# Kernel tuning notes

Hardware: AMD Instinct MI355X
Metric: run time of the kernel (lower is better)

## Reference

```python
import jax, jax.numpy as jnp
import numpy as np

EPS = 1e-6

def _layernorm(x, gamma, beta):
    # normalize over last dim (head_dim)
    mean = x.mean(axis=-1, keepdims=True)
    var = x.var(axis=-1, keepdims=True)
    return gamma * (x - mean) * jax.lax.rsqrt(var + EPS) + beta

def setup_inputs() -> dict:
    key = jax.random.key(0)
    ks = jax.random.split(key, 6)
    B, N, C, H = 2, 2048, 1024, 16
    Dh = C // H
    x = jax.random.normal(ks[0], (B, N, C), dtype=jnp.float32)
    qkv_w = jax.random.normal(ks[1], (C, 3 * C), dtype=jnp.float32) * (1.0 / np.sqrt(C))
    q_gamma = jnp.ones((Dh,), jnp.float32)
    q_beta = jnp.zeros((Dh,), jnp.float32)
    k_gamma = jnp.ones((Dh,), jnp.float32)
    k_beta = jnp.zeros((Dh,), jnp.float32)
    proj_w = jax.random.normal(ks[2], (C, C), dtype=jnp.float32) * (1.0 / np.sqrt(C))
    proj_b = jnp.zeros((C,), jnp.float32)
    return {"x": x, "qkv_w": qkv_w, "q_gamma": q_gamma, "q_beta": q_beta,
            "k_gamma": k_gamma, "k_beta": k_beta, "proj_w": proj_w, "proj_b": proj_b}

def reference(x, qkv_w, q_gamma, q_beta, k_gamma, k_beta, proj_w, proj_b):
    B, N, C = x.shape
    H = 16
    Dh = C // H
    scale = Dh ** -0.5
    qkv = x @ qkv_w                                   # [B,N,3C]
    qkv = qkv.reshape(B, N, 3, H, Dh)
    q = qkv[:, :, 0].transpose(0, 2, 1, 3)            # [B,H,N,Dh]
    k = qkv[:, :, 1].transpose(0, 2, 1, 3)
    v = qkv[:, :, 2].transpose(0, 2, 1, 3)
    q = _layernorm(q, q_gamma, q_beta)
    k = _layernorm(k, k_gamma, k_beta)
    attn = jnp.einsum('bhnd,bhmd->bhnm', q, k) * scale
    attn = jax.nn.softmax(attn, axis=-1)
    out = jnp.einsum('bhnm,bhmd->bhnd', attn, v)      # [B,H,N,Dh]
    out = out.transpose(0, 2, 1, 3).reshape(B, N, C)
    return out @ proj_w + proj_b
```

## Files before the change

### kernel.cpp

```cpp
#include <hip/hip_runtime.h>

typedef unsigned short u16;
typedef unsigned int u32;
typedef float f32x4 __attribute__((ext_vector_type(4)));
typedef float f32x16 __attribute__((ext_vector_type(16)));
typedef short s16x8 __attribute__((ext_vector_type(8)));

#define B_ 2
#define N_ 2048
#define C_ 1024
#define H_ 16
#define BN_ (B_*N_)

#define EXP2F(x) __builtin_amdgcn_exp2f(x)

__device__ __forceinline__ u16 f2bf(float f) {
  union { float f; unsigned u; } c; c.f = f;
  unsigned u = c.u;
  u = (u + 0x7fffu + ((u >> 16) & 1u)) >> 16;
  return (u16)u;
}
__device__ __forceinline__ float bf2f(u16 h) {
  union { unsigned u; float f; } c; c.u = ((unsigned)h) << 16;
  return c.f;
}
__device__ __forceinline__ u32 pack2(float lo, float hi) {
  u32 r;
  asm("v_cvt_pk_bf16_f32 %0, %1, %2" : "=v"(r) : "v"(lo), "v"(hi));
  return r;
}
__device__ __forceinline__ void plswap(u32& a, u32& b) {
  asm volatile("v_permlane32_swap_b32 %0, %1" : "+v"(a), "+v"(b));
}
__device__ __forceinline__ void gload16(const u16* g, u16* l) {
  __builtin_amdgcn_global_load_lds(
      (const __attribute__((address_space(1))) unsigned*)g,
      (__attribute__((address_space(3))) unsigned*)l, 16, 0, 0);
}

__global__ __launch_bounds__(256) void k_prep(const float* __restrict__ x,
                                              u16* __restrict__ xb,
                                              const float* __restrict__ qkv_w,
                                              u16* __restrict__ wqkvT,
                                              const float* __restrict__ proj_w,
                                              u16* __restrict__ wprojT) {
  __shared__ float t[32][33];
  int bid = blockIdx.x;
  int tid = threadIdx.x;
  if (bid < 4096) {
    int i = bid * 256 + tid;
    float4 v = ((const float4*)x)[i];
    ushort4 r;
    r.x = f2bf(v.x); r.y = f2bf(v.y); r.z = f2bf(v.z); r.w = f2bf(v.w);
    ((ushort4*)xb)[i] = r;
    return;
  }
  const float* W; u16* Wt; int R, Cc, bx, by;
  if (bid < 7168) {
    int b = bid - 4096;
    bx = b % 96; by = b / 96;
    W = qkv_w; Wt = wqkvT; R = C_; Cc = 3 * C_;
  } else {
    int b = bid - 7168;
    bx = b & 31; by = b >> 5;
    W = proj_w; Wt = wprojT; R = C_; Cc = C_;
  }
  int tx = tid & 31, ty = tid >> 5;
  int c0 = bx * 32, r0 = by * 32;
#pragma unroll
  for (int i = 0; i < 4; ++i)
    t[ty + i * 8][tx] = W[(long)(r0 + ty + i * 8) * Cc + c0 + tx];
  __syncthreads();
#pragma unroll
  for (int i = 0; i < 4; ++i)
    Wt[(long)(c0 + ty + i * 8) * R + r0 + tx] = f2bf(t[tx][ty + i * 8]);
}

__global__ __launch_bounds__(256) void k_gemm_qkv_ln(const u16* __restrict__ A,
                                                     const u16* __restrict__ Bt,
                                                     const float* __restrict__ qg,
                                                     const float* __restrict__ qbeta,
                                                     const float* __restrict__ kg,
                                                     const float* __restrict__ kbeta,
                                                     u16* __restrict__ Qh,
                                                     u16* __restrict__ Kh,
                                                     u16* __restrict__ Vt) {
  const int K = C_;
  __shared__ u16 smem[32768];
  int tid = threadIdx.x;
  int w = tid >> 6, l = tid & 63;
  int l15 = l & 15, lhi = l >> 4;
  int wm = w >> 1, wn = w & 1;
  int rowA = l >> 3;
  int colA = ((l & 7) ^ (rowA & 7)) * 8;
  int x0 = (lhi ^ (l15 & 7)) * 8;
  int x1 = ((4 + lhi) ^ (l15 & 7)) * 8;
  const u16* Ab = A + (long)blockIdx.y * 128 * K;
  const u16* Bb = Bt + (long)blockIdx.x * 128 * K;
  f32x4 acc[4][4];
#pragma unroll
  for (int m = 0; m < 4; ++m)
#pragma unroll
    for (int n = 0; n < 4; ++n)
      acc[m][n] = (f32x4){0.f, 0.f, 0.f, 0.f};

  auto STAGE = [&](int k0, int bi) {
    u16* at = smem + bi * 8192;
    u16* bt = smem + 16384 + bi * 8192;
#pragma unroll
    for (int i = 0; i < 4; ++i) {
      int ci = i * 4 + w;
      gload16(Ab + (long)(ci * 8 + rowA) * K + k0 + colA, &at[ci * 512]);
      gload16(Bb + (long)(ci * 8 + rowA) * K + k0 + colA, &bt[ci * 512]);
    }
  };

  const int NS = K / 64;
  STAGE(0, 0);
  for (int t = 0; t < NS; ++t) {
    __builtin_amdgcn_s_barrier();
    if (t + 1 < NS) {
      STAGE((t + 1) * 64, (t + 1) & 1);
      asm volatile("s_waitcnt vmcnt(8)" ::: "memory");
    } else {
      asm volatile("s_waitcnt vmcnt(0)" ::: "memory");
    }
    __builtin_amdgcn_s_barrier();
    const u16* at = smem + (t & 1) * 8192;
    const u16* bt = smem + 16384 + (t & 1) * 8192;
#pragma unroll
    for (int kk = 0; kk < 2; ++kk) {
      int xo = kk ? x1 : x0;
      s16x8 af[4], bfr[4];
#pragma unroll
      for (int m = 0; m < 4; ++m)
        af[m] = *(const s16x8*)&at[(wm * 64 + m * 16 + l15) * 64 + xo];
#pragma unroll
      for (int n = 0; n < 4; ++n)
        bfr[n] = *(const s16x8*)&bt[(wn * 64 + n * 16 + l15) * 64 + xo];
#pragma unroll
      for (int m = 0; m < 4; ++m)
#pragma unroll
        for (int n = 0; n < 4; ++n)
          acc[m][n] = __builtin_amdgcn_mfma_f32_16x16x32_bf16(af[m], bfr[n], acc[m][n], 0, 0, 0);
    }
  }

  int cb = blockIdx.x * 128 + wn * 64;
  int s = cb >> 10;
  int h = (cb & 1023) >> 6;
  int rowbase = blockIdx.y * 128 + wm * 64;

  if (s == 2) {
    __syncthreads();
    u16* tbuf = smem + w * 4608;
    u32* tb32 = (u32*)tbuf;
#pragma unroll
    for (int m = 0; m < 4; ++m)
#pragma unroll
      for (int n = 0; n < 4; ++n) {
        int d = n * 16 + l15;
#pragma unroll
        for (int r = 0; r < 4; r += 2)
          tb32[d * 36 + m * 8 + lhi * 2 + (r >> 1)] =
              pack2(acc[m][n][r], acc[m][n][r + 1]);
      }
    int b = rowbase >> 11;
    int nnb = rowbase & (N_ - 1);
    int bhv = b * H_ + h;
    int ch = (l & 7) * 8;
#pragma unroll
    for (int i = 0; i < 8; ++i) {
      int dl = i * 8 + (l >> 3);
      s16x8 vv = *(const s16x8*)&tbuf[dl * 72 + ch];
      *(s16x8*)&Vt[(long)(bhv * 64 + dl) * N_ + nnb + ch] = vv;
    }
  } else {
    const float* g = (s == 0) ? qg : kg;
    const float* be = (s == 0) ? qbeta : kbeta;
    u16* Oh = (s == 0) ? Qh : Kh;
    float sc = (s == 0) ? 0.125f * 1.44269504089f : 1.f;
    float gv[4], bv[4];
#pragma unroll
    for (int n = 0; n < 4; ++n) { gv[n] = g[n * 16 + l15]; bv[n] = be[n * 16 + l15]; }
#pragma unroll
    for (int m = 0; m < 4; ++m) {
#pragma unroll
      for (int r = 0; r < 4; ++r) {
        float t = (acc[m][0][r] + acc[m][1][r]) + (acc[m][2][r] + acc[m][3][r]);
        t += __shfl_xor(t, 1); t += __shfl_xor(t, 2);
        t += __shfl_xor(t, 4); t += __shfl_xor(t, 8);
        float mean = t * (1.f / 64.f);
        float v0 = acc[m][0][r] - mean, v1 = acc[m][1][r] - mean;
        float v2 = acc[m][2][r] - mean, v3 = acc[m][3][r] - mean;
        float q2 = (v0 * v0 + v1 * v1) + (v2 * v2 + v3 * v3);
        q2 += __shfl_xor(q2, 1); q2 += __shfl_xor(q2, 2);
        q2 += __shfl_xor(q2, 4); q2 += __shfl_xor(q2, 8);
        float rs = rsqrtf(q2 * (1.f / 64.f) + 1e-6f);
        int row = rowbase + m * 16 + lhi * 4 + r;
        int b = row >> 11, nn = row & (N_ - 1);
        long ob = ((long)(b * H_ + h) * N_ + nn) * 64;
        float vv[4] = {v0, v1, v2, v3};
#pragma unroll
        for (int n = 0; n < 4; ++n)
          Oh[ob + n * 16 + l15] = f2bf(sc * (gv[n] * vv[n] * rs + bv[n]));
      }
    }
  }
}

__global__ __launch_bounds__(256) void k_gemm_proj(const u16* __restrict__ A,
                                                   const u16* __restrict__ Bt,
                                                   float* __restrict__ Cout,
                                                   const float* __restrict__ bias,
                                                   int M, int N, int K) {
  __shared__ u16 a_t[2][128 * 64];
  __shared__ u16 b_t[2][64 * 64];
  int tid = threadIdx.x;
  int w = tid >> 6, l = tid & 63;
  int l15 = l & 15, lhi = l >> 4;
  int rowA = l >> 3;
  int colA = ((l & 7) ^ (rowA & 7)) * 8;
  int x0 = (lhi ^ (l15 & 7)) * 8;
  int x1 = ((4 + lhi) ^ (l15 & 7)) * 8;
  const u16* Ab = A + (long)blockIdx.y * 128 * K;
  const u16* Bb = Bt + (long)blockIdx.x * 64 * K;
  f32x4 acc[2][4];
#pragma unroll
  for (int m = 0; m < 2; ++m)
#pragma unroll
    for (int n = 0; n < 4; ++n)
      acc[m][n] = (f32x4){0.f, 0.f, 0.f, 0.f};

  auto STAGE = [&](int k0, int bi) {
#pragma unroll
    for (int i = 0; i < 4; ++i) {
      int ci = i * 4 + w;
      gload16(Ab + (long)(ci * 8 + rowA) * K + k0 + colA, &a_t[bi][ci * 512]);
    }
#pragma unroll
    for (int i = 0; i < 2; ++i) {
      int ci = i * 4 + w;
      gload16(Bb + (long)(ci * 8 + rowA) * K + k0 + colA, &b_t[bi][ci * 512]);
    }
  };

  const int NS = 1024 / 64;
  STAGE(0, 0);
  for (int t = 0; t < NS; ++t) {
    __builtin_amdgcn_s_barrier();
    if (t + 1 < NS) {
      STAGE((t + 1) * 64, (t + 1) & 1);
      asm volatile("s_waitcnt vmcnt(6)" ::: "memory");
    } else {
      asm volatile("s_waitcnt vmcnt(0)" ::: "memory");
    }
    __builtin_amdgcn_s_barrier();
    const u16* at = a_t[t & 1];
    const u16* bt = b_t[t & 1];
#pragma unroll
    for (int kk = 0; kk < 2; ++kk) {
      int xo = kk ? x1 : x0;
      s16x8 af[2], bfr[4];
#pragma unroll
      for (int m = 0; m < 2; ++m)
        af[m] = *(const s16x8*)&at[(w * 32 + m * 16 + l15) * 64 + xo];
#pragma unroll
      for (int n = 0; n < 4; ++n)
        bfr[n] = *(const s16x8*)&bt[(n * 16 + l15) * 64 + xo];
#pragma unroll
      for (int m = 0; m < 2; ++m)
#pragma unroll
        for (int n = 0; n < 4; ++n)
          acc[m][n] = __builtin_amdgcn_mfma_f32_16x16x32_bf16(af[m], bfr[n], acc[m][n], 0, 0, 0);
    }
  }
#pragma unroll
  for (int m = 0; m < 2; ++m) {
#pragma unroll
    for (int n = 0; n < 4; ++n) {
      int col = blockIdx.x * 64 + n * 16 + l15;
#pragma unroll
      for (int r = 0; r < 4; ++r) {
        int row = blockIdx.y * 128 + w * 32 + m * 16 + lhi * 4 + r;
        Cout[(long)row * N + col] = acc[m][n][r] + bias[col];
      }
    }
  }
}

__global__ __launch_bounds__(512, 4) void k_attn(const u16* __restrict__ Qh,
                                                 const u16* __restrict__ Kh,
                                                 const u16* __restrict__ Vt,
                                                 u16* __restrict__ O) {
  __shared__ u16 k_t[2][2][64 * 64];
  __shared__ u16 v_t[2][2][64 * 64];
  int tid = threadIdx.x;
  int w = tid >> 6, l = tid & 63;
  int half = w >> 2, wq = w & 3;
  int l31 = l & 31, hi = l >> 5;
  int id = blockIdx.x;
  int swz = (id & 7) * 64 + (id >> 3);
  int bh = swz >> 4, qb = swz & 15;
  int b = bh >> 4, h = bh & 15;
  const u16* Qb = Qh + ((long)bh * N_ + qb * 128 + wq * 32) * 64;
  const u16* Kb = Kh + ((long)bh * N_ + half * 1024) * 64;
  const u16* Vb = Vt + (long)bh * 64 * N_ + half * 1024;

  s16x8 qf[4];
#pragma unroll
  for (int j = 0; j < 4; ++j)
    qf[j] = *(const s16x8*)&Qb[l31 * 64 + j * 16 + hi * 8];

  f32x16 acc0, acc1;
#pragma unroll
  for (int i = 0; i < 16; ++i) { acc0[i] = 0.f; acc1[i] = 0.f; }
  float lsum = 0.f;

  int off[2][4];
#pragma unroll
  for (int t = 0; t < 2; ++t)
#pragma unroll
    for (int j = 0; j < 4; ++j)
      off[t][j] = (t * 32 + l31) * 64 + (((j * 2 + hi) ^ (l & 7)) * 8);

  int srow = l >> 3;
  int scol = ((l & 7) ^ srow) * 8;

  auto STAGE = [&](int kt, int bi) {
#pragma unroll
    for (int i = 0; i < 2; ++i) {
      int ci = i * 4 + wq;
      gload16(Kb + (long)(kt + ci * 8 + srow) * 64 + scol, &k_t[half][bi][ci * 512]);
      gload16(Vb + (long)(ci * 8 + srow) * N_ + kt + scol, &v_t[half][bi][ci * 512]);
    }
  };

  const int NT = 16;
  STAGE(0, 0);

  for (int t = 0; t < NT; ++t) {
    __builtin_amdgcn_s_barrier();
    if (t + 1 < NT) {
      STAGE((t + 1) * 64, (t + 1) & 1);
      asm volatile("s_waitcnt vmcnt(4)" ::: "memory");
    } else {
      asm volatile("s_waitcnt vmcnt(0)" ::: "memory");
    }
    __builtin_amdgcn_s_barrier();
    const u16* kb = k_t[half][t & 1];
    const u16* vb = v_t[half][t & 1];

    f32x16 s0, s1;
#pragma unroll
    for (int i = 0; i < 16; ++i) { s0[i] = 0.f; s1[i] = 0.f; }
    __builtin_amdgcn_s_setprio(1);
#pragma unroll
    for (int j = 0; j < 4; ++j) {
      s16x8 kf0 = *(const s16x8*)&kb[off[0][j]];
      s0 = __builtin_amdgcn_mfma_f32_32x32x16_bf16(kf0, qf[j], s0, 0, 0, 0);
      s16x8 kf1 = *(const s16x8*)&kb[off[1][j]];
      s1 = __builtin_amdgcn_mfma_f32_32x32x16_bf16(kf1, qf[j], s1, 0, 0, 0);
    }
    __builtin_amdgcn_s_setprio(0);

#pragma unroll
    for (int i = 0; i < 16; ++i) {
      s0[i] = EXP2F(s0[i]);
      s1[i] = EXP2F(s1[i]);
    }
    f32x16 sm;
#pragma unroll
    for (int i = 0; i < 16; ++i) sm[i] = s0[i] + s1[i];
#pragma unroll
    for (int i = 0; i < 8; ++i) sm[i] += sm[i + 8];
#pragma unroll
    for (int i = 0; i < 4; ++i) sm[i] += sm[i + 4];
    lsum += (sm[0] + sm[1]) + (sm[2] + sm[3]);

    s16x8 pa[4];
#pragma unroll
    for (int g = 0; g < 4; ++g) {
      const f32x16& sv = (g < 2) ? s0 : s1;
      int o = (g & 1) * 8;
      u32 a = pack2(sv[o + 0], sv[o + 1]);
      u32 bb = pack2(sv[o + 4], sv[o + 5]);
      u32 c = pack2(sv[o + 2], sv[o + 3]);
      u32 d = pack2(sv[o + 6], sv[o + 7]);
      plswap(a, bb);
      plswap(c, d);
      union { u32 u[4]; s16x8 v; } fr;
      fr.u[0] = a; fr.u[1] = c; fr.u[2] = bb; fr.u[3] = d;
      pa[g] = fr.v;
    }

    __builtin_amdgcn_s_setprio(1);
#pragma unroll
    for (int j = 0; j < 4; ++j) {
      s16x8 vf0 = *(const s16x8*)&vb[off[0][j]];
      acc0 = __builtin_amdgcn_mfma_f32_32x32x16_bf16(pa[j], vf0, acc0, 0, 0, 0);
      s16x8 vf1 = *(const s16x8*)&vb[off[1][j]];
      acc1 = __builtin_amdgcn_mfma_f32_32x32x16_bf16(pa[j], vf1, acc1, 0, 0, 0);
    }
    __builtin_amdgcn_s_setprio(0);
  }

  lsum += __shfl_xor(lsum, 32);

  __syncthreads();
  float* mbuf = (float*)&k_t[0][0][0];
  float* ml   = (float*)&v_t[0][0][0];

  if (half == 1) {
    if (hi == 0) ml[wq * 32 + l31] = lsum;
#pragma unroll
    for (int r = 0; r < 16; ++r) {
      mbuf[((wq * 32 + r) * 64) + l] = acc0[r];
      mbuf[((wq * 32 + 16 + r) * 64) + l] = acc1[r];
    }
  }
  __syncthreads();

  if (half == 0) {
    float s_b = ml[wq * 32 + l31];
    float lstar = lsum + s_b;
    int lsi = __float_as_int(lstar);
#pragma unroll
    for (int r = 0; r < 16; ++r) {
      int ql = (r & 3) + 8 * (r >> 2) + 4 * hi;
      float ls = __int_as_float(__builtin_amdgcn_ds_bpermute(ql << 2, lsi));
      float o0 = acc0[r] + mbuf[((wq * 32 + r) * 64) + l];
      float o1 = acc1[r] + mbuf[((wq * 32 + 16 + r) * 64) + l];
      float inv = 1.f / ls;
      int q = qb * 128 + wq * 32 + ql;
      long ob = ((long)(b * N_ + q) * H_ + h) * 64 + l31;
      O[ob] = f2bf(o0 * inv);
      O[ob + 32] = f2bf(o1 * inv);
    }
  }
}

extern "C" void kernel_launch(void* const* d_in, const int* in_sizes, int n_in,
                              void* d_out, int out_size, void* d_ws, size_t ws_size,
                              hipStream_t stream) {
  const float* x      = (const float*)d_in[0];
  const float* qkv_w  = (const float*)d_in[1];
  const float* q_g    = (const float*)d_in[2];
  const float* q_b    = (const float*)d_in[3];
  const float* k_g    = (const float*)d_in[4];
  const float* k_b    = (const float*)d_in[5];
  const float* proj_w = (const float*)d_in[6];
  const float* proj_b = (const float*)d_in[7];
  float* out = (float*)d_out;

  char* ws = (char*)d_ws;
  u16* xb     = (u16*)(ws + 0);
  u16* wqkvT  = (u16*)(ws + 8388608);
  u16* wprojT = (u16*)(ws + 14680064);
  u16* Qh     = (u16*)(ws + 16777216);
  u16* Kh     = (u16*)(ws + 25165824);
  u16* Vt     = (u16*)(ws + 41943040);
  u16* attnO  = xb;

  k_prep<<<8192, 256, 0, stream>>>(x, xb, qkv_w, wqkvT, proj_w, wprojT);
  k_gemm_qkv_ln<<<dim3(24, 32), 256, 0, stream>>>(xb, wqkvT, q_g, q_b, k_g, k_b, Qh, Kh, Vt);
  k_attn<<<512, 512, 0, stream>>>(Qh, Kh, Vt, attnO);
  k_gemm_proj<<<dim3(16, 32), 256, 0, stream>>>(attnO, wprojT, out, proj_b, BN_, C_, C_);
}
```

Before: 112.8 us.

## Drop key-split in attention kernel; each wave processes full key range

The attention kernel no longer splits the key sequence across two half-blocks of 4 waves each. It now uses 256 threads per block, and each wave iterates over all 32 key tiles. This removes the cross-half reduction through shared memory, its two __syncthreads, and halves the LDS footprint, which could raise occupancy. In exchange each block runs a serial loop twice as long with half the waves, which gives less latency hiding per block. There is also a cosmetic change to the projection GEMM's LDS indexing.

```diff
diff --git a/kernel.cpp b/kernel.cpp
--- a/kernel.cpp
+++ b/kernel.cpp
@@ -264,7 +264,7 @@
       s16x8 af[2], bfr[4];
 #pragma unroll
       for (int m = 0; m < 2; ++m)
-        af[m] = *(const s16x8*)&at[(w * 32 + m * 16 + l15) * 64 + xo];
+        af[m] = *(const s16x8*)&a_t[t & 1][(w * 32 + m * 16 + l15) * 64 + xo];
 #pragma unroll
       for (int n = 0; n < 4; ++n)
         bfr[n] = *(const s16x8*)&bt[(n * 16 + l15) * 64 + xo];
@@ -273,6 +273,7 @@
 #pragma unroll
         for (int n = 0; n < 4; ++n)
           acc[m][n] = __builtin_amdgcn_mfma_f32_16x16x32_bf16(af[m], bfr[n], acc[m][n], 0, 0, 0);
+      (void)at;
     }
   }
 #pragma unroll
@@ -289,23 +290,22 @@
   }
 }
 
-__global__ __launch_bounds__(512, 4) void k_attn(const u16* __restrict__ Qh,
+__global__ __launch_bounds__(256, 4) void k_attn(const u16* __restrict__ Qh,
                                                  const u16* __restrict__ Kh,
                                                  const u16* __restrict__ Vt,
                                                  u16* __restrict__ O) {
-  __shared__ u16 k_t[2][2][64 * 64];
-  __shared__ u16 v_t[2][2][64 * 64];
+  __shared__ u16 k_t[2][64 * 64];
+  __shared__ u16 v_t[2][64 * 64];
   int tid = threadIdx.x;
   int w = tid >> 6, l = tid & 63;
-  int half = w >> 2, wq = w & 3;
   int l31 = l & 31, hi = l >> 5;
   int id = blockIdx.x;
   int swz = (id & 7) * 64 + (id >> 3);
   int bh = swz >> 4, qb = swz & 15;
   int b = bh >> 4, h = bh & 15;
-  const u16* Qb = Qh + ((long)bh * N_ + qb * 128 + wq * 32) * 64;
-  const u16* Kb = Kh + ((long)bh * N_ + half * 1024) * 64;
-  const u16* Vb = Vt + (long)bh * 64 * N_ + half * 1024;
+  const u16* Qb = Qh + ((long)bh * N_ + qb * 128 + w * 32) * 64;
+  const u16* Kb = Kh + (long)bh * N_ * 64;
+  const u16* Vb = Vt + (long)bh * 64 * N_;
 
   s16x8 qf[4];
 #pragma unroll
@@ -330,13 +330,13 @@
   auto STAGE = [&](int kt, int bi) {
 #pragma unroll
     for (int i = 0; i < 2; ++i) {
-      int ci = i * 4 + wq;
-      gload16(Kb + (long)(kt + ci * 8 + srow) * 64 + scol, &k_t[half][bi][ci * 512]);
-      gload16(Vb + (long)(ci * 8 + srow) * N_ + kt + scol, &v_t[half][bi][ci * 512]);
+      int ci = i * 4 + w;
+      gload16(Kb + (long)(kt + ci * 8 + srow) * 64 + scol, &k_t[bi][ci * 512]);
+      gload16(Vb + (long)(ci * 8 + srow) * N_ + kt + scol, &v_t[bi][ci * 512]);
     }
   };
 
-  const int NT = 16;
+  const int NT = N_ / 64;
   STAGE(0, 0);
 
   for (int t = 0; t < NT; ++t) {
@@ -348,8 +348,8 @@
       asm volatile("s_waitcnt vmcnt(0)" ::: "memory");
     }
     __builtin_amdgcn_s_barrier();
-    const u16* kb = k_t[half][t & 1];
-    const u16* vb = v_t[half][t & 1];
+    const u16* kb = k_t[t & 1];
+    const u16* vb = v_t[t & 1];
 
     f32x16 s0, s1;
 #pragma unroll
@@ -406,37 +406,16 @@
   }
 
   lsum += __shfl_xor(lsum, 32);
-
-  __syncthreads();
-  float* mbuf = (float*)&k_t[0][0][0];
-  float* ml   = (float*)&v_t[0][0][0];
-
-  if (half == 1) {
-    if (hi == 0) ml[wq * 32 + l31] = lsum;
-#pragma unroll
-    for (int r = 0; r < 16; ++r) {
-      mbuf[((wq * 32 + r) * 64) + l] = acc0[r];
-      mbuf[((wq * 32 + 16 + r) * 64) + l] = acc1[r];
-    }
-  }
-  __syncthreads();
-
-  if (half == 0) {
-    float s_b = ml[wq * 32 + l31];
-    float lstar = lsum + s_b;
-    int lsi = __float_as_int(lstar);
-#pragma unroll
-    for (int r = 0; r < 16; ++r) {
-      int ql = (r & 3) + 8 * (r >> 2) + 4 * hi;
-      float ls = __int_as_float(__builtin_amdgcn_ds_bpermute(ql << 2, lsi));
-      float o0 = acc0[r] + mbuf[((wq * 32 + r) * 64) + l];
-      float o1 = acc1[r] + mbuf[((wq * 32 + 16 + r) * 64) + l];
-      float inv = 1.f / ls;
-      int q = qb * 128 + wq * 32 + ql;
-      long ob = ((long)(b * N_ + q) * H_ + h) * 64 + l31;
-      O[ob] = f2bf(o0 * inv);
-      O[ob + 32] = f2bf(o1 * inv);
-    }
+  int lsi = __float_as_int(lsum);
+#pragma unroll
+  for (int r = 0; r < 16; ++r) {
+    int ql = (r & 3) + 8 * (r >> 2) + 4 * hi;
+    float ls = __int_as_float(__builtin_amdgcn_ds_bpermute(ql << 2, lsi));
+    float inv = 1.f / ls;
+    int q = qb * 128 + w * 32 + ql;
+    long ob = ((long)(b * N_ + q) * H_ + h) * 64 + l31;
+    O[ob] = f2bf(acc0[r] * inv);
+    O[ob + 32] = f2bf(acc1[r] * inv);
   }
 }
 
@@ -464,6 +443,6 @@
 
   k_prep<<<8192, 256, 0, stream>>>(x, xb, qkv_w, wqkvT, proj_w, wprojT);
   k_gemm_qkv_ln<<<dim3(24, 32), 256, 0, stream>>>(xb, wqkvT, q_g, q_b, k_g, k_b, Qh, Kh, Vt);
-  k_attn<<<512, 512, 0, stream>>>(Qh, Kh, Vt, attnO);
+  k_attn<<<512, 256, 0, stream>>>(Qh, Kh, Vt, attnO);
   k_gemm_proj<<<dim3(16, 32), 256, 0, stream>>>(attnO, wprojT, out, proj_b, BN_, C_, C_);
 }
```

New measurement: 116.4 us. 1.03x slower.
